# Performance work log

Measured on AMD Instinct MI355X. Metric: run time of the kernel, lower is better.

The kernel has to match this reference:

```python
import jax, jax.numpy as jnp
import numpy as np

# Fixed multi-scale pyramid (H, W) per level -- static config, closed over.
SPATIAL_SHAPES = [(100, 100), (50, 50), (25, 25), (13, 13)]
D_MODEL, N_HEADS, N_LEVELS, N_POINTS = 256, 8, 4, 4
C_HEAD = D_MODEL // N_HEADS
B = 2
NUM_KEYS = sum(h * w for h, w in SPATIAL_SHAPES)  # 13294
NUM_QUERIES = NUM_KEYS


def setup_inputs() -> dict:
    key = jax.random.key(0)
    ks = jax.random.split(key, 12)
    d = D_MODEL
    return {
        "query": jax.random.normal(ks[0], (B, NUM_QUERIES, d), jnp.float32),
        "reference_points": jax.random.uniform(ks[1], (B, NUM_QUERIES, N_LEVELS, 2), jnp.float32),
        "input_flatten": jax.random.normal(ks[2], (B, NUM_KEYS, d), jnp.float32),
        "Wv": jax.random.normal(ks[3], (d, d), jnp.float32) * 0.02,
        "bv": jnp.zeros((d,), jnp.float32),
        "Ws": jax.random.normal(ks[4], (d, N_HEADS * N_LEVELS * N_POINTS * 2), jnp.float32) * 0.01,
        "bs": jax.random.normal(ks[5], (N_HEADS * N_LEVELS * N_POINTS * 2,), jnp.float32),
        "Wa": jax.random.normal(ks[6], (d, N_HEADS * N_LEVELS * N_POINTS), jnp.float32) * 0.02,
        "ba": jnp.zeros((N_HEADS * N_LEVELS * N_POINTS,), jnp.float32),
        "Wo": jax.random.normal(ks[7], (d, d), jnp.float32) * 0.02,
        "bo": jnp.zeros((d,), jnp.float32),
    }


def _bilinear_sample(v, grid, H, W):
    """torch.F.grid_sample(mode='bilinear', padding_mode='zeros', align_corners=False).
    v: (N, H, W, C); grid: (N, M, 2) with (x, y) in [-1, 1]. Returns (N, M, C)."""
    x = (grid[..., 0] + 1.0) * (W * 0.5) - 0.5
    y = (grid[..., 1] + 1.0) * (H * 0.5) - 0.5
    x0 = jnp.floor(x)
    y0 = jnp.floor(y)
    dx = x - x0
    dy = y - y0
    x0i = x0.astype(jnp.int32)
    y0i = y0.astype(jnp.int32)
    vflat = v.reshape(v.shape[0], H * W, v.shape[-1])

    def gather(xi, yi):
        valid = (xi >= 0) & (xi < W) & (yi >= 0) & (yi < H)
        idx = jnp.clip(yi, 0, H - 1) * W + jnp.clip(xi, 0, W - 1)  # (N, M)
        g = jnp.take_along_axis(vflat, idx[..., None], axis=1)
        return g * valid[..., None]

    v00 = gather(x0i, y0i)
    v10 = gather(x0i + 1, y0i)
    v01 = gather(x0i, y0i + 1)
    v11 = gather(x0i + 1, y0i + 1)
    return (v00 * ((1 - dx) * (1 - dy))[..., None]
            + v10 * (dx * (1 - dy))[..., None]
            + v01 * ((1 - dx) * dy)[..., None]
            + v11 * (dx * dy)[..., None])


def _ms_deform_attn(value, sampling_locations, attention_weights):
    # value: (B, NK, H, Ch); loc: (B, NQ, H, L, P, 2); w: (B, NQ, H, L, P)
    grids = 2.0 * sampling_locations - 1.0
    splits = np.cumsum([h * w for h, w in SPATIAL_SHAPES])[:-1]
    value_list = jnp.split(value, splits, axis=1)
    acc = 0.0
    for lvl, (H, W) in enumerate(SPATIAL_SHAPES):
        # (B, H*W, heads, Ch) -> (B*heads, H, W, Ch)
        v_l = value_list[lvl].reshape(B, H, W, N_HEADS, C_HEAD)
        v_l = v_l.transpose(0, 3, 1, 2, 4).reshape(B * N_HEADS, H, W, C_HEAD)
        # (B, NQ, heads, P, 2) -> (B*heads, NQ*P, 2)
        g_l = grids[:, :, :, lvl].transpose(0, 2, 1, 3, 4).reshape(B * N_HEADS, -1, 2)
        samp = _bilinear_sample(v_l, g_l, H, W)  # (B*heads, NQ*P, Ch)
        samp = samp.reshape(B, N_HEADS, -1, N_POINTS, C_HEAD)
        w_l = attention_weights[:, :, :, lvl].transpose(0, 2, 1, 3)  # (B, heads, NQ, P)
        acc = acc + jnp.einsum("bhqpc,bhqp->bhqc", samp, w_l)
    return acc.transpose(0, 2, 1, 3).reshape(B, -1, D_MODEL)  # (B, NQ, d_model)


def reference(query, reference_points, input_flatten, Wv, bv, Ws, bs, Wa, ba, Wo, bo):
    value = (input_flatten @ Wv + bv).reshape(B, NUM_KEYS, N_HEADS, C_HEAD)
    offsets = (query @ Ws + bs).reshape(B, NUM_QUERIES, N_HEADS, N_LEVELS, N_POINTS, 2)
    attw = jax.nn.softmax(
        (query @ Wa + ba).reshape(B, NUM_QUERIES, N_HEADS, N_LEVELS * N_POINTS), axis=-1
    ).reshape(B, NUM_QUERIES, N_HEADS, N_LEVELS, N_POINTS)
    # NOTE: module divides by [H, W] (not [W, H]) -- replicated faithfully.
    normalizer = jnp.asarray(SPATIAL_SHAPES, jnp.float32)  # (L, 2) = (H, W)
    normalizer = jnp.clip(normalizer, 1.0)
    loc = reference_points[:, :, None, :, None, :] + offsets / normalizer[None, None, None, :, None, :]
    out = _ms_deform_attn(value, loc, attw)
    return out @ Wo + bo
```

## Files before the change

kernel.cpp:

```cpp
#include <hip/hip_runtime.h>
#include <hip/hip_bf16.h>
#include <hip/hip_fp16.h>
#include <math.h>

#define B_  2
#define NQ  13294
#define NK  13294
#define M_  (B_ * NK)
#define MT  32
#define GX  ((M_ + MT - 1) / MT)

typedef __bf16 bf16x8 __attribute__((ext_vector_type(8)));
typedef float f32x4 __attribute__((ext_vector_type(4)));

static __device__ __forceinline__ f32x4 mfma16(bf16x8 a, bf16x8 b, f32x4 c) {
  return __builtin_amdgcn_mfma_f32_16x16x32_bf16(a, b, c, 0, 0, 0);
}

static __device__ __forceinline__ void pack_one(
    const float* __restrict__ W1, const float* __restrict__ W2,
    int N1, int Ntot, __hip_bfloat16* __restrict__ out, int g) {
  int lane = g & 63;
  int n_sub = (g >> 6) & 3;
  int kt = (g >> 8) & 7;
  int bn = g >> 11;
  int n = bn * 64 + n_sub * 16 + (lane & 15);
  int k0 = kt * 32 + (lane >> 4) * 8;
  const float* src; int nn, Ns;
  if (n < N1) { src = W1; nn = n; Ns = N1; }
  else        { src = W2; nn = n - N1; Ns = Ntot - N1; }
  bf16x8 v;
#pragma unroll
  for (int j = 0; j < 8; ++j) v[j] = (__bf16)src[(size_t)(k0 + j) * Ns + nn];
  *(bf16x8*)(out + (size_t)g * 8) = v;
}

__global__ __launch_bounds__(256) void pack_all(
    const float* __restrict__ Wv, const float* __restrict__ Ws,
    const float* __restrict__ Wa, const float* __restrict__ Wo,
    __hip_bfloat16* __restrict__ wv_p, __hip_bfloat16* __restrict__ wsa_p,
    __hip_bfloat16* __restrict__ wo_p) {
  const int b = blockIdx.x, t = threadIdx.x;
  if (b < 32)       pack_one(Wv, Wv, 256, 256, wv_p,  b * 256 + t);
  else if (b < 80)  pack_one(Ws, Wa, 256, 384, wsa_p, (b - 32) * 256 + t);
  else              pack_one(Wo, Wo, 256, 256, wo_p,  (b - 80) * 256 + t);
}

#define CSTR 68

__global__ __launch_bounds__(128) void gemm_mt(
    const float* __restrict__ inpf, const float* __restrict__ query,
    const bf16x8* __restrict__ wv_p, const bf16x8* __restrict__ wsa_p,
    const float* __restrict__ bv, const float* __restrict__ bs,
    const float* __restrict__ ba,
    __hip_bfloat16* __restrict__ value, __half* __restrict__ params) {
  __shared__ bf16x8 As[8 * 2 * 64];
  __shared__ float  Cs[2 * MT * CSTR];

  const int t = threadIdx.x;
  const int bm = blockIdx.x * MT;
  const int lane = t & 63, wid = t >> 6;
  const int mode = blockIdx.y;

  {
    const int r = t >> 2;
    const int row = bm + r;
    const int sm = r >> 4;
    const int lb = r & 15;
    const bool ok = row < M_;
    const float* Af = (mode == 0) ? inpf : query;
    const float* ap = Af + (size_t)row * 256 + (t & 3) * 64;
#pragma unroll
    for (int gi = 0; gi < 8; ++gi) {
      float4 u = make_float4(0.f,0.f,0.f,0.f), v = make_float4(0.f,0.f,0.f,0.f);
      if (ok) { u = *(const float4*)(ap + gi * 8); v = *(const float4*)(ap + gi * 8 + 4); }
      bf16x8 w;
      w[0]=(__bf16)u.x; w[1]=(__bf16)u.y; w[2]=(__bf16)u.z; w[3]=(__bf16)u.w;
      w[4]=(__bf16)v.x; w[5]=(__bf16)v.y; w[6]=(__bf16)v.z; w[7]=(__bf16)v.w;
      int k8 = (t & 3) * 8 + gi;
      As[((k8 >> 2) * 2 + sm) * 64 + lb + ((k8 & 3) << 4)] = w;
    }
  }
  __syncthreads();

  const bf16x8* Bp = (mode == 0) ? wv_p : wsa_p;
  const int NB = (mode == 1) ? 6 : 4;
  float* Cw = &Cs[wid * MT * CSTR];

  for (int nb = wid; nb < NB; nb += 2) {
    const int colbase = nb * 64;
    const bf16x8* bpn = Bp + (size_t)nb * 2048;

    f32x4 acc[2][4] = {};
#pragma unroll
    for (int kt = 0; kt < 8; ++kt) {
      bf16x8 a0 = As[(kt * 2 + 0) * 64 + lane];
      bf16x8 a1 = As[(kt * 2 + 1) * 64 + lane];
#pragma unroll
      for (int n = 0; n < 4; ++n) {
        bf16x8 b = bpn[(kt * 4 + n) * 64 + lane];
        acc[0][n] = mfma16(a0, b, acc[0][n]);
        acc[1][n] = mfma16(a1, b, acc[1][n]);
      }
    }

#pragma unroll
    for (int m = 0; m < 2; ++m)
#pragma unroll
      for (int n = 0; n < 4; ++n)
#pragma unroll
        for (int rg = 0; rg < 4; ++rg)
          Cw[(m * 16 + (lane >> 4) * 4 + rg) * CSTR + n * 16 + (lane & 15)] = acc[m][n][rg];

    if (mode == 0) {
#pragma unroll
      for (int p = 0; p < 4; ++p) {
        const int r = (lane >> 3) + p * 8;
        const int c = (lane & 7) * 8;
        const int row = bm + r;
        float4 u = *(float4*)&Cw[r * CSTR + c];
        float4 v = *(float4*)&Cw[r * CSTR + c + 4];
        const float* bias = bv + colbase + c;
        bf16x8 o;
        o[0]=(__bf16)(u.x+bias[0]); o[1]=(__bf16)(u.y+bias[1]);
        o[2]=(__bf16)(u.z+bias[2]); o[3]=(__bf16)(u.w+bias[3]);
        o[4]=(__bf16)(v.x+bias[4]); o[5]=(__bf16)(v.y+bias[5]);
        o[6]=(__bf16)(v.z+bias[6]); o[7]=(__bf16)(v.w+bias[7]);
        if (row < M_)
          *(bf16x8*)(value + (size_t)row * 256 + colbase + c) = o;
      }
    } else {
#pragma unroll
      for (int p = 0; p < 8; ++p) {
        const int r = (lane >> 4) + p * 4;
        const int c = (lane & 15) * 4;
        const int row = bm + r;
        const int col = colbase + c;
        float4 u = *(float4*)&Cw[r * CSTR + c];
        const float* bias = (col < 256) ? (bs + col) : (ba + col - 256);
        u.x += bias[0]; u.y += bias[1]; u.z += bias[2]; u.w += bias[3];
        if (row < M_) {
          __half2 h0 = __floats2half2_rn(u.x, u.y);
          __half2 h1 = __floats2half2_rn(u.z, u.w);
          uint2 st;
          st.x = *(unsigned int*)&h0;
          st.y = *(unsigned int*)&h1;
          *(uint2*)(params + (size_t)row * 384 + col) = st;
        }
      }
    }
  }
}

#define CS 65
#define REGH (64 * CS)

__global__ __launch_bounds__(256) void sampler(
    const float* __restrict__ refp, const __half* __restrict__ params,
    const __hip_bfloat16* __restrict__ value, const bf16x8* __restrict__ wo_p,
    const float* __restrict__ bo, float* __restrict__ outp) {
  __shared__ unsigned int combo[2 * REGH];

  const int t = threadIdx.x;
  const int q0 = blockIdx.x * 16;
  const int bb = blockIdx.y;

  const int cqi = t >> 5;
  const int chh = (t >> 2) & 7;
  const int cl  = t & 3;

  const int lane = t & 63;
  const int wid  = t >> 6;
  const int q2   = lane >> 5;
  const int gh   = (lane >> 2) & 7;
  const int gs   = lane & 3;
  const char* vb = (const char*)value;
  const unsigned int voff0 = (unsigned int)bb * (NK * 512u) + (unsigned)(gh * 64 + gs * 16);

  const float DIMF[4]  = {100.f, 50.f, 25.f, 13.f};
  const int   LSTART[4] = {0, 10000, 12500, 13125};
  const float dimf  = DIMF[cl];
  const int   Wd    = (int)dimf;
  const int   lbase = LSTART[cl];

  for (int qc = 0; qc < 16; qc += 8) {
    unsigned int* reg = combo + ((qc >> 3) & 1) * REGH;
    {
      const int q = q0 + qc + cqi;
      const bool valid = q < NQ;
      const size_t row = (size_t)bb * NQ + (valid ? q : 0);
      const __half* pr = params + row * 384;

      union { uint4 u[2]; __half h[16]; } LG;
      LG.u[0] = *(const uint4*)(pr + 256 + chh * 16);
      LG.u[1] = *(const uint4*)(pr + 256 + chh * 16 + 8);
      float lgf[16];
#pragma unroll
      for (int j = 0; j < 16; ++j) lgf[j] = __half2float(LG.h[j]);
      float m = lgf[0];
#pragma unroll
      for (int j = 1; j < 16; ++j) m = fmaxf(m, lgf[j]);
      float s = 0.f;
#pragma unroll
      for (int j = 0; j < 16; ++j) s += __expf(lgf[j] - m);
      const float inv = valid ? 1.f / s : 0.f;

      const float rx = refp[(row * 4 + cl) * 2 + 0];
      const float ry = refp[(row * 4 + cl) * 2 + 1];
      union { uint4 u; __half h[8]; } OF;
      OF.u = *(const uint4*)(pr + chh * 32 + cl * 8);
      unsigned int* cb = &reg[(cqi * 8 + chh) * CS + cl * 16];

#pragma unroll
      for (int p = 0; p < 4; ++p) {
        const float wa = __expf(lgf[cl * 4 + p] - m) * inv;
        const float x = rx * dimf + __half2float(OF.h[p * 2 + 0]) - 0.5f;
        const float y = ry * dimf + __half2float(OF.h[p * 2 + 1]) - 0.5f;
        const float xf = floorf(x), yf = floorf(y);
        const float dx = x - xf, dy = y - yf;
        const int x0 = (int)xf, y0 = (int)yf;
        float w00 = (1.f - dx) * (1.f - dy) * wa;
        float w10 = dx * (1.f - dy) * wa;
        float w01 = (1.f - dx) * dy * wa;
        float w11 = dx * dy * wa;
        int i0, i1, i2, i3, xi, yi;
        xi = x0;     yi = y0;
        if (xi >= 0 && xi < Wd && yi >= 0 && yi < Wd) i0 = lbase + yi * Wd + xi; else { i0 = 0; w00 = 0.f; }
        xi = x0 + 1; yi = y0;
        if (xi >= 0 && xi < Wd && yi >= 0 && yi < Wd) i1 = lbase + yi * Wd + xi; else { i1 = 0; w10 = 0.f; }
        xi = x0;     yi = y0 + 1;
        if (xi >= 0 && xi < Wd && yi >= 0 && yi < Wd) i2 = lbase + yi * Wd + xi; else { i2 = 0; w01 = 0.f; }
        xi = x0 + 1; yi = y0 + 1;
        if (xi >= 0 && xi < Wd && yi >= 0 && yi < Wd) i3 = lbase + yi * Wd + xi; else { i3 = 0; w11 = 0.f; }
        cb[p * 4 + 0] = ((__float_as_uint(w00) + 0x8000u) & 0xffff0000u) | (unsigned)i0;
        cb[p * 4 + 1] = ((__float_as_uint(w10) + 0x8000u) & 0xffff0000u) | (unsigned)i1;
        cb[p * 4 + 2] = ((__float_as_uint(w01) + 0x8000u) & 0xffff0000u) | (unsigned)i2;
        cb[p * 4 + 3] = ((__float_as_uint(w11) + 0x8000u) & 0xffff0000u) | (unsigned)i3;
      }
    }
    __syncthreads();

    {
      const int qw = wid * 2 + q2;
      const int rr = qw * 8 + gh;
      const unsigned int* cb = &reg[rr * CS];
      float a0=0.f,a1=0.f,a2=0.f,a3=0.f,a4=0.f,a5=0.f,a6=0.f,a7=0.f;
#pragma unroll 8
      for (int e = 0; e < 64; ++e) {
        const unsigned int u = cb[e];
        const float w = __uint_as_float(u & 0xffff0000u);
        const unsigned int voff = voff0 + ((u & 0xffffu) << 9);
        const uint4 v = *(const uint4*)(vb + (size_t)voff);
        a0 += w * __uint_as_float(v.x << 16);
        a1 += w * __uint_as_float(v.x & 0xffff0000u);
        a2 += w * __uint_as_float(v.y << 16);
        a3 += w * __uint_as_float(v.y & 0xffff0000u);
        a4 += w * __uint_as_float(v.z << 16);
        a5 += w * __uint_as_float(v.z & 0xffff0000u);
        a6 += w * __uint_as_float(v.w << 16);
        a7 += w * __uint_as_float(v.w & 0xffff0000u);
      }
      bf16x8 o;
      o[0]=(__bf16)a0; o[1]=(__bf16)a1; o[2]=(__bf16)a2; o[3]=(__bf16)a3;
      o[4]=(__bf16)a4; o[5]=(__bf16)a5; o[6]=(__bf16)a6; o[7]=(__bf16)a7;
      const int s = (4 - (rr & 3)) & 3;
      *(bf16x8*)(&reg[rr * CS + s + gs * 4]) = o;
    }
  }
  __syncthreads();

  {
    const unsigned int* abase = combo + ((lane >> 3) & 1) * REGH
                              + (lane & 7) * (8 * CS) + (lane >> 4) * 4;
    const bf16x8* bpn = wo_p + (size_t)wid * 2048;
    f32x4 oacc[4] = {};
#pragma unroll
    for (int kt = 0; kt < 8; ++kt) {
      const int s = (4 - (kt & 3)) & 3;
      bf16x8 a = *(const bf16x8*)(abase + kt * CS + s);
#pragma unroll
      for (int n = 0; n < 4; ++n)
        oacc[n] = mfma16(a, bpn[(kt * 4 + n) * 64 + lane], oacc[n]);
    }
#pragma unroll
    for (int n = 0; n < 4; ++n) {
      const int col = wid * 64 + n * 16 + (lane & 15);
      const float bias = bo[col];
#pragma unroll
      for (int rg = 0; rg < 4; ++rg) {
        const int ql = (lane >> 4) * 4 + rg;
        const int q = q0 + ql;
        if (q < NQ)
          outp[((size_t)bb * NQ + q) * 256 + col] = oacc[n][rg] + bias;
      }
    }
  }
}

extern "C" void kernel_launch(void* const* d_in, const int* in_sizes, int n_in,
                              void* d_out, int out_size, void* d_ws, size_t ws_size,
                              hipStream_t stream) {
  const float* query = (const float*)d_in[0];
  const float* refp  = (const float*)d_in[1];
  const float* inpf  = (const float*)d_in[2];
  const float* Wv    = (const float*)d_in[3];
  const float* bv    = (const float*)d_in[4];
  const float* Ws    = (const float*)d_in[5];
  const float* bs    = (const float*)d_in[6];
  const float* Wa    = (const float*)d_in[7];
  const float* ba    = (const float*)d_in[8];
  const float* Wo    = (const float*)d_in[9];
  const float* bo    = (const float*)d_in[10];
  float* out = (float*)d_out;

  char* w = (char*)d_ws;
  __hip_bfloat16* value  = (__hip_bfloat16*)w;            w += (size_t)M_ * 256 * 2;
  __half*         params = (__half*)w;                    w += (size_t)M_ * 384 * 2;
  __hip_bfloat16* wv_p   = (__hip_bfloat16*)w;            w += 256 * 256 * 2;
  __hip_bfloat16* wsa_p  = (__hip_bfloat16*)w;            w += 256 * 384 * 2;
  __hip_bfloat16* wo_p   = (__hip_bfloat16*)w;

  pack_all<<<112, 256, 0, stream>>>(Wv, Ws, Wa, Wo, wv_p, wsa_p, wo_p);

  gemm_mt<<<dim3(GX, 2), 128, 0, stream>>>(
      inpf, query, (const bf16x8*)wv_p, (const bf16x8*)wsa_p,
      bv, bs, ba, value, params);

  dim3 sgrid((NQ + 15) / 16, B_);
  sampler<<<sgrid, 256, 0, stream>>>(refp, params, value,
                                     (const bf16x8*)wo_p, bo, out);
}
```

Measured before the change: 126.8 us.

## Reorder queries by reference-point spatial bins before sampling for cache locality

Adds a histogram, scan and scatter pass that buckets queries into a 32x32 grid by their level-0 reference point, producing a permutation. The sampler then processes queries in spatially sorted order so nearby blocks gather overlapping value rows. It also remaps block indices with an XCD-style interleave (blockIdx & 7), so each group of eight consecutive blocks covers both batches and four query ranges. This trades three extra small kernel launches, a memset and the atomic-based counting sort for better L2 hit rates on the scattered value gathers. Output rows are written back through the permutation.

```diff
diff --git a/kernel.cpp b/kernel.cpp
--- a/kernel.cpp
+++ b/kernel.cpp
@@ -44,6 +44,51 @@
   if (b < 32)       pack_one(Wv, Wv, 256, 256, wv_p,  b * 256 + t);
   else if (b < 80)  pack_one(Ws, Wa, 256, 384, wsa_p, (b - 32) * 256 + t);
   else              pack_one(Wo, Wo, 256, 256, wo_p,  (b - 80) * 256 + t);
+}
+
+static __device__ __forceinline__ int bin_of(const float* refp, int b, int q) {
+  const size_t base = (((size_t)b * NQ + q) * 4) * 2;
+  float rx = refp[base + 0], ry = refp[base + 1];
+  int bx = (int)(rx * 32.f); bx = bx < 0 ? 0 : (bx > 31 ? 31 : bx);
+  int by = (int)(ry * 32.f); by = by < 0 ? 0 : (by > 31 ? 31 : by);
+  return b * 1024 + by * 32 + bx;
+}
+
+__global__ __launch_bounds__(256) void hist_k(
+    const float* __restrict__ refp, unsigned int* __restrict__ hist) {
+  int i = blockIdx.x * 256 + threadIdx.x;
+  if (i >= 2 * NQ) return;
+  int b = i >= NQ; int q = i - b * NQ;
+  atomicAdd(&hist[bin_of(refp, b, q)], 1u);
+}
+
+__global__ __launch_bounds__(256) void scan_k(
+    const unsigned int* __restrict__ hist, unsigned int* __restrict__ cursor) {
+  __shared__ unsigned int lds[256];
+  const int t = threadIdx.x;
+  unsigned int v[8], s = 0;
+#pragma unroll
+  for (int j = 0; j < 8; ++j) { v[j] = hist[t * 8 + j]; s += v[j]; }
+  lds[t] = s; __syncthreads();
+  for (int off = 1; off < 256; off <<= 1) {
+    unsigned int x = (t >= off) ? lds[t - off] : 0u;
+    __syncthreads();
+    lds[t] += x;
+    __syncthreads();
+  }
+  unsigned int base = lds[t] - s;
+#pragma unroll
+  for (int j = 0; j < 8; ++j) { cursor[t * 8 + j] = base; base += v[j]; }
+}
+
+__global__ __launch_bounds__(256) void scatter_k(
+    const float* __restrict__ refp, unsigned int* __restrict__ cursor,
+    unsigned int* __restrict__ perm) {
+  int i = blockIdx.x * 256 + threadIdx.x;
+  if (i >= 2 * NQ) return;
+  int b = i >= NQ; int q = i - b * NQ;
+  unsigned int pos = atomicAdd(&cursor[bin_of(refp, b, q)], 1u);
+  perm[pos] = (unsigned int)q;
 }
 
 #define CSTR 68
@@ -158,12 +203,22 @@
 __global__ __launch_bounds__(256) void sampler(
     const float* __restrict__ refp, const __half* __restrict__ params,
     const __hip_bfloat16* __restrict__ value, const bf16x8* __restrict__ wo_p,
-    const float* __restrict__ bo, float* __restrict__ outp) {
+    const float* __restrict__ bo, const unsigned int* __restrict__ perm,
+    float* __restrict__ outp) {
   __shared__ unsigned int combo[2 * REGH];
+  __shared__ unsigned int qmap[16];
+
+  const int c  = blockIdx.x & 7;
+  const int kk = blockIdx.x >> 3;
+  const int bb = c >> 2;
+  const int qb = (c & 3) * 208 + kk;
+  if (qb > 830) return;
+  const int q0 = qb * 16;
 
   const int t = threadIdx.x;
-  const int q0 = blockIdx.x * 16;
-  const int bb = blockIdx.y;
+  if (t < 16)
+    qmap[t] = (q0 + t < NQ) ? perm[(size_t)bb * NQ + q0 + t] : 0xFFFFFFFFu;
+  __syncthreads();
 
   const int cqi = t >> 5;
   const int chh = (t >> 2) & 7;
@@ -186,9 +241,9 @@
   for (int qc = 0; qc < 16; qc += 8) {
     unsigned int* reg = combo + ((qc >> 3) & 1) * REGH;
     {
-      const int q = q0 + qc + cqi;
-      const bool valid = q < NQ;
-      const size_t row = (size_t)bb * NQ + (valid ? q : 0);
+      const unsigned int qreal = qmap[qc + cqi];
+      const bool valid = qreal != 0xFFFFFFFFu;
+      const size_t row = (size_t)bb * NQ + (valid ? qreal : 0);
       const __half* pr = params + row * 384;
 
       union { uint4 u[2]; __half h[16]; } LG;
@@ -289,9 +344,9 @@
 #pragma unroll
       for (int rg = 0; rg < 4; ++rg) {
         const int ql = (lane >> 4) * 4 + rg;
-        const int q = q0 + ql;
-        if (q < NQ)
-          outp[((size_t)bb * NQ + q) * 256 + col] = oacc[n][rg] + bias;
+        const unsigned int qreal = qmap[ql];
+        if (qreal != 0xFFFFFFFFu)
+          outp[((size_t)bb * NQ + qreal) * 256 + col] = oacc[n][rg] + bias;
       }
     }
   }
@@ -318,7 +373,17 @@
   __half*         params = (__half*)w;                    w += (size_t)M_ * 384 * 2;
   __hip_bfloat16* wv_p   = (__hip_bfloat16*)w;            w += 256 * 256 * 2;
   __hip_bfloat16* wsa_p  = (__hip_bfloat16*)w;            w += 256 * 384 * 2;
-  __hip_bfloat16* wo_p   = (__hip_bfloat16*)w;
+  __hip_bfloat16* wo_p   = (__hip_bfloat16*)w;            w += 256 * 256 * 2;
+  unsigned int*   hist   = (unsigned int*)w;              w += 2048 * 4;
+  unsigned int*   cursor = (unsigned int*)w;              w += 2048 * 4;
+  unsigned int*   perm   = (unsigned int*)w;
+
+  hipMemsetAsync(hist, 0, 2048 * 4, stream);
+
+  const int sg = (2 * NQ + 255) / 256;
+  hist_k<<<sg, 256, 0, stream>>>(refp, hist);
+  scan_k<<<1, 256, 0, stream>>>(hist, cursor);
+  scatter_k<<<sg, 256, 0, stream>>>(refp, cursor, perm);
 
   pack_all<<<112, 256, 0, stream>>>(Wv, Ws, Wa, Wo, wv_p, wsa_p, wo_p);
 
@@ -326,7 +391,6 @@
       inpf, query, (const bf16x8*)wv_p, (const bf16x8*)wsa_p,
       bv, bs, ba, value, params);
 
-  dim3 sgrid((NQ + 15) / 16, B_);
-  sampler<<<sgrid, 256, 0, stream>>>(refp, params, value,
-                                     (const bf16x8*)wo_p, bo, out);
-}
+  sampler<<<1664, 256, 0, stream>>>(refp, params, value,
+                                    (const bf16x8*)wo_p, bo, perm, out);
+}
```

Result: faster. 115.9 us (-8.6%).
